# Kernel optimization log

Hardware: AMD Instinct MI355X
Metric: run time of the kernel (lower is better)

Reference implementation:

```python
import jax, jax.numpy as jnp
import numpy as np

IN_C, HID, OUT = 3, 128, 256
K1, K2 = 16, 8
N = 8192


def _knn_idx(x, k):
    # x: [N, C] -> indices of k nearest neighbors (excluding self), [N, k]
    n = x.shape[0]
    sq = jnp.sum(x * x, axis=1)
    d = sq[:, None] + sq[None, :] - 2.0 * (x @ x.T)  # [N, N] squared dists
    i = jnp.arange(n)
    d = d.at[i, i].set(jnp.inf)  # loop=False: exclude self
    _, idx = jax.lax.top_k(-d, k)
    return idx


def _edge_conv(x, W1, b1, W2, b2, k):
    # DynamicEdgeConv: knn graph on x, edge feat [x_i, x_j - x_i], MLP, max aggr
    n, c = x.shape
    idx = _knn_idx(x, k)              # [N, k]
    xj = x[idx]                       # [N, k, C]
    xi = x[:, None, :]                # [N, 1, C]
    e = jnp.concatenate([jnp.broadcast_to(xi, (n, k, c)), xj - xi], axis=-1)  # [N, k, 2C]
    h = jax.nn.relu(e @ W1 + b1) @ W2 + b2  # [N, k, H]
    return jnp.max(h, axis=1)               # max aggregation -> [N, H]


def setup_inputs() -> dict:
    key = jax.random.key(0)
    ks = jax.random.split(key, 9)
    def lin(k, fan_in, fan_out):
        bound = 1.0 / np.sqrt(fan_in)
        kw, kb = jax.random.split(k)
        W = jax.random.uniform(kw, (fan_in, fan_out), jnp.float32, -bound, bound)
        b = jax.random.uniform(kb, (fan_out,), jnp.float32, -bound, bound)
        return W, b
    x = jax.random.normal(ks[0], (N, IN_C), jnp.float32)
    W1a, b1a = lin(ks[1], 2 * IN_C, HID)
    W1b, b1b = lin(ks[2], HID, HID)
    W2a, b2a = lin(ks[3], 2 * HID, OUT)
    W2b, b2b = lin(ks[4], OUT, OUT)
    return {"x": x, "W1a": W1a, "b1a": b1a, "W1b": W1b, "b1b": b1b,
            "W2a": W2a, "b2a": b2a, "W2b": W2b, "b2b": b2b}


def reference(x, W1a, b1a, W1b, b1b, W2a, b2a, W2b, b2b):
    h = _edge_conv(x, W1a, b1a, W1b, b1b, K1)   # [N, HID]
    out = _edge_conv(h, W2a, b2a, W2b, b2b, K2)  # [N, OUT]
    return out
```

## Files before the change

### kernel.cpp

```cpp
#include <hip/hip_runtime.h>
#include <math.h>

constexpr int NPTS  = 8192;
constexpr int HIDC  = 128;
constexpr int OUTC2 = 256;
constexpr int PQC   = 512;
constexpr int KK1   = 16;
constexpr int KK2   = 8;

typedef __attribute__((ext_vector_type(8))) short short8;
typedef __attribute__((ext_vector_type(4))) float f32x4;

__device__ __forceinline__ f32x4 mfma16(short8 a, short8 b, f32x4 c) {
  return __builtin_amdgcn_mfma_f32_16x16x32_bf16(a, b, c, 0, 0, 0);
}

__device__ __forceinline__ void async_ld16(void* lds, const void* g) {
  __builtin_amdgcn_global_load_lds(
      (const __attribute__((address_space(1))) unsigned int*)g,
      (__attribute__((address_space(3))) unsigned int*)lds, 16, 0, 0);
}

#define CEU(a, b) { unsigned _t = (a) < (b) ? (a) : (b); (b) = (a) < (b) ? (b) : (a); (a) = _t; }

__device__ __forceinline__ void topk8_batch4(unsigned (&kk)[KK2],
                                             unsigned b0, unsigned b1,
                                             unsigned b2, unsigned b3) {
  CEU(b0, b1); CEU(b2, b3); CEU(b0, b2); CEU(b1, b3); CEU(b1, b2);
  if (b0 < kk[7]) {
    kk[4] = kk[4] < b3 ? kk[4] : b3;
    kk[5] = kk[5] < b2 ? kk[5] : b2;
    kk[6] = kk[6] < b1 ? kk[6] : b1;
    kk[7] = kk[7] < b0 ? kk[7] : b0;
    CEU(kk[0], kk[4]); CEU(kk[1], kk[5]); CEU(kk[2], kk[6]); CEU(kk[3], kk[7]);
    CEU(kk[0], kk[2]); CEU(kk[1], kk[3]); CEU(kk[4], kk[6]); CEU(kk[5], kk[7]);
    CEU(kk[0], kk[1]); CEU(kk[2], kk[3]); CEU(kk[4], kk[5]); CEU(kk[6], kk[7]);
  }
}

template <int K>
__device__ __forceinline__ void ins_lex(float (&kf)[K], int (&ki)[K], float v, int j) {
  bool ins = (v < kf[K - 1]) || (v == kf[K - 1] && j < ki[K - 1]);
  if (ins) {
    kf[K - 1] = v; ki[K - 1] = j;
    #pragma unroll
    for (int p = K - 1; p > 0; --p) {
      float fa = kf[p - 1], fb = kf[p];
      int   ia = ki[p - 1], ib = ki[p];
      bool sw = (fb < fa) || (fb == fa && ib < ia);
      kf[p - 1] = sw ? fb : fa; ki[p - 1] = sw ? ib : ia;
      kf[p]     = sw ? fa : fb; ki[p]     = sw ? ia : ib;
    }
  }
}

__device__ __forceinline__ unsigned short bf16_rn(float x) {
  unsigned int u = __float_as_uint(x);
  unsigned int r = u + 0x7fffu + ((u >> 16) & 1u);
  return (unsigned short)(r >> 16);
}

__global__ void pack_x_kernel(const float* __restrict__ x, float4* __restrict__ x4) {
  int i = blockIdx.x * blockDim.x + threadIdx.x;
  if (i < NPTS) {
    float a = x[3 * i], b = x[3 * i + 1], c = x[3 * i + 2];
    x4[i] = make_float4(a, b, c, a * a + b * b + c * c);
  }
}

__global__ void prep_w1f_kernel(const float* __restrict__ W1,
                                unsigned short* __restrict__ WcFhi,
                                unsigned short* __restrict__ WcFlo) {
  int idx = blockIdx.x * 256 + threadIdx.x;
  int k = idx >> 9, c = idx & 511;
  float wh = W1[(size_t)(HIDC + k) * OUTC2 + (c & 255)];
  float w = (c < OUTC2) ? (W1[(size_t)k * OUTC2 + c] - wh) : wh;
  unsigned short hi = bf16_rn(w);
  float fh = __uint_as_float(((unsigned int)hi) << 16);
  unsigned short lo = bf16_rn(w - fh);
  const int nt = c >> 4, ct = c & 15;
  const int s = k >> 5, kg = (k >> 3) & 3, e = k & 7;
  const size_t fidx = ((size_t)(s * 32 + nt) * 64 + (kg * 16 + ct)) * 8 + e;
  WcFhi[fidx] = hi;
  WcFlo[fidx] = lo;
}

__global__ void prep_w1b_kernel(const float* __restrict__ W,
                                unsigned short* __restrict__ Fhi,
                                unsigned short* __restrict__ Flo) {
  const int c = blockIdx.x;
  const int k = threadIdx.x;
  float w = W[(size_t)k * HIDC + c];
  unsigned short hi = bf16_rn(w);
  float fh = __uint_as_float(((unsigned int)hi) << 16);
  unsigned short lo = bf16_rn(w - fh);
  const int nt = c >> 4, ct = c & 15;
  const int s = k >> 5, kg = (k >> 3) & 3, e = k & 7;
  const size_t idx = ((size_t)(s * 8 + nt) * 64 + (kg * 16 + ct)) * 8 + e;
  Fhi[idx] = hi;
  Flo[idx] = lo;
}

__global__ void prep_w2_kernel(const float* __restrict__ W2,
                               unsigned short* __restrict__ W2Fhi,
                               unsigned short* __restrict__ W2Flo) {
  const int c = blockIdx.x;
  const int k = threadIdx.x;
  float w = W2[(size_t)k * OUTC2 + c];
  unsigned short hi = bf16_rn(w);
  float fh = __uint_as_float(((unsigned int)hi) << 16);
  unsigned short lo = bf16_rn(w - fh);
  const int nt = c >> 4, ct = c & 15;
  const int s  = k >> 5, kg = (k >> 3) & 3, e = k & 7;
  const int lane = kg * 16 + ct;
  const size_t idx = ((size_t)(s * 16 + nt) * 64 + lane) * 8 + e;
  W2Fhi[idx] = hi;
  W2Flo[idx] = lo;
}

__global__ __launch_bounds__(256) void knn3_kernel(const float4* __restrict__ X4,
                                                   int* __restrict__ idx_out) {
  const int tid  = threadIdx.x;
  const int lane = tid & 63;
  const int wv   = __builtin_amdgcn_readfirstlane(tid >> 6);
  const int qA   = blockIdx.x * 8 + wv * 2;
  const int qB   = qA + 1;

  const float4 qa = X4[qA];
  const float4 qb = X4[qB];

  unsigned kkA[KK2], kkB[KK2];
  #pragma unroll
  for (int k = 0; k < KK2; ++k) { kkA[k] = 0xFFFFFFFFu; kkB[k] = 0xFFFFFFFFu; }

  for (int c = 0; c < NPTS / 256; ++c) {
    const int j = c * 256 + lane * 4;
    float4 p[4];
    #pragma unroll
    for (int t = 0; t < 4; ++t) p[t] = X4[j + t];

    unsigned ka[4], kb[4];
    #pragma unroll
    for (int t = 0; t < 4; ++t) {
      float dA = fmaxf(qa.w + p[t].w - 2.f * (qa.x * p[t].x + qa.y * p[t].y + qa.z * p[t].z), 0.f);
      float dB = fmaxf(qb.w + p[t].w - 2.f * (qb.x * p[t].x + qb.y * p[t].y + qb.z * p[t].z), 0.f);
      ka[t] = (__float_as_uint(dA) & 0xFFFFE000u) | (unsigned)(j + t);
      kb[t] = (__float_as_uint(dB) & 0xFFFFE000u) | (unsigned)(j + t);
      if (j + t == qA) ka[t] = 0xFFFFFFFFu;
      if (j + t == qB) kb[t] = 0xFFFFFFFFu;
    }
    topk8_batch4(kkA, ka[0], ka[1], ka[2], ka[3]);
    topk8_batch4(kkB, kb[0], kb[1], kb[2], kb[3]);
  }

  float kfA[KK2], kfB[KK2]; int kjA[KK2], kjB[KK2];
  #pragma unroll
  for (int k = 0; k < KK2; ++k) {
    kfA[k] = INFINITY; kjA[k] = 0x7fffffff;
    kfB[k] = INFINITY; kjB[k] = 0x7fffffff;
  }
  #pragma unroll
  for (int k = 0; k < KK2; ++k) {
    int j = (int)(kkA[k] & 0x1FFFu);
    float4 pj = X4[j];
    float d = qa.w + pj.w - 2.f * (qa.x * pj.x + qa.y * pj.y + qa.z * pj.z);
    if (kkA[k] == 0xFFFFFFFFu) { d = INFINITY; j = 0x7fffffff; }
    ins_lex<KK2>(kfA, kjA, d, j);
  }
  #pragma unroll
  for (int k = 0; k < KK2; ++k) {
    int j = (int)(kkB[k] & 0x1FFFu);
    float4 pj = X4[j];
    float d = qb.w + pj.w - 2.f * (qb.x * pj.x + qb.y * pj.y + qb.z * pj.z);
    if (kkB[k] == 0xFFFFFFFFu) { d = INFINITY; j = 0x7fffffff; }
    ins_lex<KK2>(kfB, kjB, d, j);
  }

  #pragma unroll
  for (int k = 0; k < KK1; ++k) {
    float mf = kfA[0]; int mj = kjA[0];
    #pragma unroll
    for (int m = 1; m <= 32; m <<= 1) {
      float of = __shfl_xor(mf, m, 64);
      int   oj = __shfl_xor(mj, m, 64);
      bool g = (of < mf) || (of == mf && oj < mj);
      mf = g ? of : mf; mj = g ? oj : mj;
    }
    const bool won = (kfA[0] == mf) && (kjA[0] == mj);
    if (won) {
      idx_out[(size_t)qA * KK1 + k] = mj;
      #pragma unroll
      for (int p = 0; p < KK2 - 1; ++p) { kfA[p] = kfA[p + 1]; kjA[p] = kjA[p + 1]; }
      kfA[KK2 - 1] = INFINITY; kjA[KK2 - 1] = 0x7fffffff;
    }
  }
  #pragma unroll
  for (int k = 0; k < KK1; ++k) {
    float mf = kfB[0]; int mj = kjB[0];
    #pragma unroll
    for (int m = 1; m <= 32; m <<= 1) {
      float of = __shfl_xor(mf, m, 64);
      int   oj = __shfl_xor(mj, m, 64);
      bool g = (of < mf) || (of == mf && oj < mj);
      mf = g ? of : mf; mj = g ? oj : mj;
    }
    const bool won = (kfB[0] == mf) && (kjB[0] == mj);
    if (won) {
      idx_out[(size_t)qB * KK1 + k] = mj;
      #pragma unroll
      for (int p = 0; p < KK2 - 1; ++p) { kfB[p] = kfB[p + 1]; kjB[p] = kjB[p + 1]; }
      kfB[KK2 - 1] = INFINITY; kjB[KK2 - 1] = 0x7fffffff;
    }
  }
}

__global__ __launch_bounds__(512) void edgeconv1_kernel(
    const float* __restrict__ X, const int* __restrict__ knn,
    const float* __restrict__ W1, const float* __restrict__ b1,
    const unsigned short* __restrict__ W1bFhi, const unsigned short* __restrict__ W1bFlo,
    const float* __restrict__ b2,
    float* __restrict__ H, unsigned short* __restrict__ Hhi,
    unsigned short* __restrict__ Hlo, float* __restrict__ SQ2) {
  __shared__ __align__(16) unsigned short Ghi[128 * HIDC];
  __shared__ __align__(16) unsigned short Glo[128 * HIDC];
  __shared__ __align__(16) unsigned short Bs[2][2][4096];
  __shared__ float xjs[8][KK1][3];
  __shared__ float xis[8][3];
  const int tid  = threadIdx.x;
  const int lane = tid & 63;
  const int wv   = __builtin_amdgcn_readfirstlane(tid >> 6);
  const int p    = blockIdx.x * 8 + wv;

  if (lane < KK1) {
    int j = knn[p * KK1 + lane];
    xjs[wv][lane][0] = X[3 * j]; xjs[wv][lane][1] = X[3 * j + 1]; xjs[wv][lane][2] = X[3 * j + 2];
  } else if (lane < KK1 + 3) {
    xis[wv][lane - KK1] = X[3 * p + lane - KK1];
  }
  __syncthreads();

  {
    const int ch0 = lane * 2;
    float2 w1r[6];
    #pragma unroll
    for (int c = 0; c < 6; ++c)
      w1r[c] = make_float2(W1[c * HIDC + ch0], W1[c * HIDC + ch0 + 1]);
    const float2 b1v = make_float2(b1[ch0], b1[ch0 + 1]);
    const float xi0 = xis[wv][0], xi1 = xis[wv][1], xi2 = xis[wv][2];
    const float base0 = b1v.x + xi0 * w1r[0].x + xi1 * w1r[1].x + xi2 * w1r[2].x;
    const float base1 = b1v.y + xi0 * w1r[0].y + xi1 * w1r[1].y + xi2 * w1r[2].y;
    #pragma unroll
    for (int e = 0; e < KK1; ++e) {
      float dx = xjs[wv][e][0] - xi0, dy = xjs[wv][e][1] - xi1, dz = xjs[wv][e][2] - xi2;
      float v0 = fmaxf(base0 + dx * w1r[3].x + dy * w1r[4].x + dz * w1r[5].x, 0.f);
      float v1 = fmaxf(base1 + dx * w1r[3].y + dy * w1r[4].y + dz * w1r[5].y, 0.f);
      unsigned short h0 = bf16_rn(v0), h1s = bf16_rn(v1);
      unsigned short l0 = bf16_rn(v0 - __uint_as_float(((unsigned)h0) << 16));
      unsigned short l1 = bf16_rn(v1 - __uint_as_float(((unsigned)h1s) << 16));
      const int r   = wv * 16 + e;
      const int off = r * 256 + (((ch0 >> 3) ^ (r & 7)) << 4) + ((ch0 & 7) << 1);
      *(ushort2*)((char*)Ghi + off) = make_ushort2(h0, h1s);
      *(ushort2*)((char*)Glo + off) = make_ushort2(l0, l1);
    }
  }

  auto stageB = [&](int buf, int s) {
    const size_t go = (size_t)s * 4096 + (size_t)wv * 512 + (size_t)lane * 8;
    async_ld16((char*)&Bs[buf][0][0] + wv * 1024, W1bFhi + go);
    async_ld16((char*)&Bs[buf][1][0] + wv * 1024, W1bFlo + go);
  };

  stageB(0, 0);
  asm volatile("s_waitcnt vmcnt(0)" ::: "memory");
  __syncthreads();

  const int col = lane & 15;
  const int kg  = lane >> 4;
  const int ar  = wv * 16 + col;
  const int abase = ar * 256;

  f32x4 acc[8];
  #pragma unroll
  for (int n = 0; n < 8; ++n) acc[n] = (f32x4){0.f, 0.f, 0.f, 0.f};

  for (int s = 0; s < 4; ++s) {
    const int cur = s & 1;
    if (s + 1 < 4) stageB(cur ^ 1, s + 1);
    const int asl = (((s * 4 + kg) ^ (ar & 7)) << 4);
    short8 ghi = *(const short8*)((const char*)Ghi + abase + asl);
    short8 glo = *(const short8*)((const char*)Glo + abase + asl);
    #pragma unroll
    for (int n = 0; n < 8; ++n) {
      const int bo = (n * 64 + lane) * 16;
      short8 bhi = *(const short8*)((const char*)&Bs[cur][0][0] + bo);
      short8 blo = *(const short8*)((const char*)&Bs[cur][1][0] + bo);
      acc[n] = mfma16(ghi, bhi, acc[n]);
      acc[n] = mfma16(ghi, blo, acc[n]);
      acc[n] = mfma16(glo, bhi, acc[n]);
    }
    asm volatile("s_waitcnt vmcnt(0)" ::: "memory");
    __syncthreads();
  }

  float sq = 0.f;
  float hv[8];
  #pragma unroll
  for (int n = 0; n < 8; ++n) {
    float m = fmaxf(fmaxf(acc[n][0], acc[n][1]), fmaxf(acc[n][2], acc[n][3]));
    m = fmaxf(m, __shfl_xor(m, 16, 64));
    m = fmaxf(m, __shfl_xor(m, 32, 64));
    m += b2[n * 16 + col];
    hv[n] = m;
    sq += m * m;
  }
  if (kg == 0) {
    #pragma unroll
    for (int n = 0; n < 8; ++n) {
      const int ch = n * 16 + col;
      H[(size_t)p * HIDC + ch] = hv[n];
      unsigned short hb = bf16_rn(hv[n]);
      float fh = __uint_as_float(((unsigned)hb) << 16);
      Hhi[(size_t)p * HIDC + ch] = hb;
      Hlo[(size_t)p * HIDC + ch] = bf16_rn(hv[n] - fh);
    }
  }
  #pragma unroll
  for (int m2 = 1; m2 <= 8; m2 <<= 1) sq += __shfl_xor(sq, m2, 64);
  if (lane == 0) SQ2[p] = sq;
}

__global__ __launch_bounds__(512) void gemm_pq_kernel(
    const unsigned short* __restrict__ Hhi, const unsigned short* __restrict__ Hlo,
    const unsigned short* __restrict__ WcFhi, const unsigned short* __restrict__ WcFlo,
    const float* __restrict__ b1, float* __restrict__ PQ) {
  __shared__ __align__(16) unsigned short Ahi[64 * HIDC];
  __shared__ __align__(16) unsigned short Alo[64 * HIDC];
  __shared__ __align__(16) unsigned short Bsl[2][2][8192];
  const int tid  = threadIdx.x;
  const int lane = tid & 63;
  const int wv   = __builtin_amdgcn_readfirstlane(tid >> 6);
  const int mb   = blockIdx.x >> 1;
  const int ns   = blockIdx.x & 1;
  const int r0   = mb * 64;

  #pragma unroll
  for (int i = 0; i < 2; ++i) {
    const int srow = wv * 8 + i * 4 + (lane >> 4);
    const int sslt = (lane & 15) ^ (srow & 7);
    const size_t go = (size_t)(r0 + srow) * HIDC + sslt * 8;
    async_ld16((char*)Ahi + (wv * 8 + i * 4) * 256, Hhi + go);
    async_ld16((char*)Alo + (wv * 8 + i * 4) * 256, Hlo + go);
  }
  auto stageB = [&](int buf, int s) {
    #pragma unroll
    for (int i = 0; i < 2; ++i) {
      const size_t go = (size_t)(s * 32 + ns * 16) * 512 + (size_t)wv * 1024 + i * 512 + lane * 8;
      async_ld16((char*)&Bsl[buf][0][0] + wv * 2048 + i * 1024, WcFhi + go);
      async_ld16((char*)&Bsl[buf][1][0] + wv * 2048 + i * 1024, WcFlo + go);
    }
  };
  stageB(0, 0);
  asm volatile("s_waitcnt vmcnt(0)" ::: "memory");
  __syncthreads();

  const int col = lane & 15;
  const int kg  = lane >> 4;
  const int mt  = wv & 3;
  const int nh  = wv >> 2;
  const int ar  = mt * 16 + col;
  const int abase = ar * 256;

  f32x4 acc[8];
  #pragma unroll
  for (int n = 0; n < 8; ++n) acc[n] = (f32x4){0.f, 0.f, 0.f, 0.f};

  for (int s = 0; s < 4; ++s) {
    const int cur = s & 1;
    if (s + 1 < 4) stageB(cur ^ 1, s + 1);
    const int asl = (((s * 4 + kg) ^ (ar & 7)) << 4);
    short8 ahi8 = *(const short8*)((const char*)Ahi + abase + asl);
    short8 alo8 = *(const short8*)((const char*)Alo + abase + asl);
    #pragma unroll
    for (int n = 0; n < 8; ++n) {
      const int ntl = nh * 8 + n;
      const int bo = (ntl * 64 + lane) * 16;
      short8 bhi = *(const short8*)((const char*)&Bsl[cur][0][0] + bo);
      short8 blo = *(const short8*)((const char*)&Bsl[cur][1][0] + bo);
      acc[n] = mfma16(ahi8, bhi, acc[n]);
      acc[n] = mfma16(ahi8, blo, acc[n]);
      acc[n] = mfma16(alo8, bhi, acc[n]);
    }
    asm volatile("s_waitcnt vmcnt(0)" ::: "memory");
    __syncthreads();
  }

  #pragma unroll
  for (int n = 0; n < 8; ++n) {
    const int cg = ns * 256 + (nh * 8 + n) * 16 + col;
    const float bb = (ns == 0) ? b1[cg] : 0.f;
    #pragma unroll
    for (int r = 0; r < 4; ++r) {
      const int row = r0 + mt * 16 + kg * 4 + r;
      PQ[(size_t)row * PQC + cg] = acc[n][r] + bb;
    }
  }
}

constexpr int JSPLIT = 16;
constexpr int JPB2   = NPTS / JSPLIT;
constexpr int NCH    = JPB2 / 16;
constexpr int CPQ    = JSPLIT * KK2;

__global__ __launch_bounds__(256) void knn128_filter_kernel(
    const unsigned short* __restrict__ Hhi, const unsigned short* __restrict__ Hlo,
    const float* __restrict__ SQ, unsigned* __restrict__ pk2) {
  __shared__ __align__(16) unsigned short As[2][2][16 * HIDC];
  const int tid  = threadIdx.x;
  const int lane = tid & 63;
  const int wv   = __builtin_amdgcn_readfirstlane(tid >> 6);
  const int qb   = blockIdx.x >> 4;
  const int js   = blockIdx.x & 15;
  const int col  = lane & 15;
  const int kg   = lane >> 4;
  const int qg   = qb * 64 + wv * 16 + col;

  short8 qhi[4], qlo[4];
  #pragma unroll
  for (int s = 0; s < 4; ++s) {
    const size_t o = (size_t)qg * HIDC + s * 32 + kg * 8;
    qhi[s] = *reinterpret_cast<const short8*>(Hhi + o);
    qlo[s] = *reinterpret_cast<const short8*>(Hlo + o);
  }
  const float sqq = SQ[qg];

  unsigned kk[KK2];
  #pragma unroll
  for (int k = 0; k < KK2; ++k) kk[k] = 0xFFFFFFFFu;

  const int jbase = js * JPB2;

  const int srow = 4 * wv + (lane >> 4);
  const int sslt = (lane & 15) ^ (srow & 7);
  auto stage = [&](int buf, int ch) {
    const size_t gofs = (size_t)(jbase + ch * 16 + srow) * HIDC + sslt * 8;
    async_ld16((char*)&As[buf][0][0] + wv * 1024, Hhi + gofs);
    async_ld16((char*)&As[buf][1][0] + wv * 1024, Hlo + gofs);
  };

  stage(0, 0);
  asm volatile("s_waitcnt vmcnt(0)" ::: "memory");
  __syncthreads();

  for (int ch = 0; ch < NCH; ++ch) {
    const int cur = ch & 1;
    if (ch + 1 < NCH) stage(cur ^ 1, ch + 1);

    const int jb = jbase + ch * 16;
    short8 ahi[4], alo[4];
    const int rowb = col * 256;
    #pragma unroll
    for (int s = 0; s < 4; ++s) {
      const int sl = ((s * 4 + kg) ^ (col & 7)) * 16;
      ahi[s] = *(const short8*)((const char*)&As[cur][0][0] + rowb + sl);
      alo[s] = *(const short8*)((const char*)&As[cur][1][0] + rowb + sl);
    }
    f32x4 sqjv = *reinterpret_cast<const f32x4*>(SQ + jb + kg * 4);

    f32x4 acc = {0.f, 0.f, 0.f, 0.f};
    #pragma unroll
    for (int s = 0; s < 4; ++s) {
      acc = mfma16(ahi[s], qhi[s], acc);
      acc = mfma16(ahi[s], qlo[s], acc);
      acc = mfma16(alo[s], qhi[s], acc);
    }
    unsigned kb[4];
    #pragma unroll
    for (int r = 0; r < 4; ++r) {
      const int jg = jb + kg * 4 + r;
      float d = fmaxf(sqq + sqjv[r] - 2.f * acc[r], 0.f);
      kb[r] = (__float_as_uint(d) & 0xFFFFE000u) | (unsigned)jg;
      if (jg == qg) kb[r] = 0xFFFFFFFFu;
    }
    topk8_batch4(kk, kb[0], kb[1], kb[2], kb[3]);
    asm volatile("s_waitcnt vmcnt(0)" ::: "memory");
    __syncthreads();
  }

  #pragma unroll
  for (int dlt = 16; dlt <= 32; dlt <<= 1) {
    unsigned ok[KK2];
    #pragma unroll
    for (int k = 0; k < KK2; ++k) ok[k] = __shfl_xor((int)kk[k], dlt, 64);
    topk8_batch4(kk, ok[0], ok[1], ok[2], ok[3]);
    topk8_batch4(kk, ok[4], ok[5], ok[6], ok[7]);
  }
  if (lane < 16) {
    const size_t base = (size_t)qg * CPQ + js * KK2;
    #pragma unroll
    for (int k = 0; k < KK2; ++k) pk2[base + k] = kk[k];
  }
}

__global__ __launch_bounds__(256) void knn_rescore_kernel(
    const float* __restrict__ H, const float* __restrict__ SQ,
    const unsigned* __restrict__ pk2, int* __restrict__ idx_out) {
  __shared__ float qrow[16][HIDC + 4];
  const int tid  = threadIdx.x;
  const int lane = tid & 63;
  const int wv   = tid >> 6;
  const int g    = lane >> 4;
  const int sl   = lane & 15;
  const int q0   = blockIdx.x * 16;
  const int qloc = wv * 4 + g;
  const int q    = q0 + qloc;

  for (int u = tid; u < 16 * 32; u += 256) {
    int r = u >> 5, c4 = u & 31;
    *(f32x4*)&qrow[r][c4 * 4] = *(const f32x4*)&H[(size_t)(q0 + r) * HIDC + c4 * 4];
  }
  __syncthreads();

  unsigned kreg[KK2];
  {
    const unsigned* src = pk2 + (size_t)q * CPQ + sl * KK2;
    uint4 a = *(const uint4*)(src);
    uint4 b = *(const uint4*)(src + 4);
    kreg[0] = a.x; kreg[1] = a.y; kreg[2] = a.z; kreg[3] = a.w;
    kreg[4] = b.x; kreg[5] = b.y; kreg[6] = b.z; kreg[7] = b.w;
  }

  unsigned ckey = 0xFFFFFFFFu;
  #pragma unroll
  for (int t = 0; t < 16; ++t) {
    unsigned m = kreg[0];
    #pragma unroll
    for (int mm = 1; mm <= 8; mm <<= 1) {
      unsigned o = (unsigned)__shfl_xor((int)m, mm, 64);
      m = o < m ? o : m;
    }
    if (t == sl) ckey = m;
    const bool won = (kreg[0] == m);
    if (won) {
      #pragma unroll
      for (int p = 0; p < KK2 - 1; ++p) kreg[p] = kreg[p + 1];
      kreg[KK2 - 1] = 0xFFFFFFFFu;
    }
  }
  const int ci = (int)(ckey & 0x1FFFu);

  const float* crow = H + (size_t)ci * HIDC;
  float dot = 0.f;
  #pragma unroll 8
  for (int c4 = 0; c4 < HIDC / 4; ++c4) {
    f32x4 qv = *(const f32x4*)&qrow[qloc][c4 * 4];
    f32x4 cv = *(const f32x4*)(crow + c4 * 4);
    dot += qv[0] * cv[0] + qv[1] * cv[1] + qv[2] * cv[2] + qv[3] * cv[3];
  }
  float d = SQ[q] + SQ[ci] - 2.f * dot;

  float kf[KK2]; int ki[KK2];
  kf[0] = d; ki[0] = ci;
  #pragma unroll
  for (int k = 1; k < KK2; ++k) { kf[k] = INFINITY; ki[k] = 0x7fffffff; }
  #pragma unroll
  for (int dlt = 1; dlt <= 8; dlt <<= 1) {
    float of[KK2]; int oi[KK2];
    #pragma unroll
    for (int k = 0; k < KK2; ++k) { of[k] = __shfl_xor(kf[k], dlt, 64); oi[k] = __shfl_xor(ki[k], dlt, 64); }
    #pragma unroll
    for (int k = 0; k < KK2; ++k) ins_lex<KK2>(kf, ki, of[k], oi[k]);
  }
  if (sl == 0) {
    #pragma unroll
    for (int k = 0; k < KK2; ++k) idx_out[(size_t)q * KK2 + k] = ki[k];
  }
}

__global__ __launch_bounds__(512) void edgeconv2_kernel(
    const float* __restrict__ PQ, const int* __restrict__ knn,
    const unsigned short* __restrict__ W2Fhi, const unsigned short* __restrict__ W2Flo,
    const float* __restrict__ b2, float* __restrict__ Out) {
  __shared__ __align__(16) unsigned short Ghi[64 * OUTC2];
  __shared__ __align__(16) unsigned short Glo[64 * OUTC2];
  __shared__ __align__(16) unsigned short Bs[2][2][8192];
  const int tid  = threadIdx.x;
  const int lane = tid & 63;
  const int wv   = __builtin_amdgcn_readfirstlane(tid >> 6);
  const int p_base = blockIdx.x * 8;

  {
    const int p   = p_base + wv;
    const int ch0 = lane * 4;
    f32x4 pv = *(const f32x4*)&PQ[(size_t)p * PQC + ch0];
    #pragma unroll
    for (int e = 0; e < KK2; ++e) {
      const int j = knn[p * KK2 + e];
      f32x4 qv = *(const f32x4*)&PQ[(size_t)j * PQC + OUTC2 + ch0];
      unsigned short hb[4], lb[4];
      #pragma unroll
      for (int c = 0; c < 4; ++c) {
        float g = fmaxf(pv[c] + qv[c], 0.f);
        hb[c] = bf16_rn(g);
        float fh = __uint_as_float(((unsigned int)hb[c]) << 16);
        lb[c] = bf16_rn(g - fh);
      }
      const int r   = wv * 8 + e;
      const int off = r * 512 + (((ch0 >> 3) ^ (r & 7)) << 4) + ((ch0 & 7) << 1);
      *(ushort4*)((char*)Ghi + off) = make_ushort4(hb[0], hb[1], hb[2], hb[3]);
      *(ushort4*)((char*)Glo + off) = make_ushort4(lb[0], lb[1], lb[2], lb[3]);
    }
  }

  auto stageB = [&](int buf, int s) {
    #pragma unroll
    for (int i = 0; i < 2; ++i) {
      const size_t go = (size_t)s * 8192 + (size_t)(wv * 2 + i) * 512 + (size_t)lane * 8;
      async_ld16((char*)&Bs[buf][0][0] + (wv * 2 + i) * 1024, W2Fhi + go);
      async_ld16((char*)&Bs[buf][1][0] + (wv * 2 + i) * 1024, W2Flo + go);
    }
  };

  stageB(0, 0);
  asm volatile("s_waitcnt vmcnt(0)" ::: "memory");
  __syncthreads();

  const int col = lane & 15;
  const int kg  = lane >> 4;
  const int mt  = wv & 3;
  const int nh  = wv >> 2;
  const int ar  = mt * 16 + col;
  const int abase = ar * 512;

  f32x4 acc[8];
  #pragma unroll
  for (int n = 0; n < 8; ++n) acc[n] = (f32x4){0.f, 0.f, 0.f, 0.f};

  for (int s = 0; s < 8; ++s) {
    const int cur = s & 1;
    if (s + 1 < 8) stageB(cur ^ 1, s + 1);

    const int asl = (((s * 4 + kg) ^ (ar & 7)) << 4);
    short8 ghi = *(const short8*)((const char*)Ghi + abase + asl);
    short8 glo = *(const short8*)((const char*)Glo + abase + asl);
    #pragma unroll
    for (int n = 0; n < 8; ++n) {
      const int nt = nh * 8 + n;
      const int bo = (nt * 64 + lane) * 16;
      short8 bhi = *(const short8*)((const char*)&Bs[cur][0][0] + bo);
      short8 blo = *(const short8*)((const char*)&Bs[cur][1][0] + bo);
      acc[n] = mfma16(ghi, bhi, acc[n]);
      acc[n] = mfma16(ghi, blo, acc[n]);
      acc[n] = mfma16(glo, bhi, acc[n]);
    }
    asm volatile("s_waitcnt vmcnt(0)" ::: "memory");
    __syncthreads();
  }

  const int pt = p_base + mt * 2 + (kg >> 1);
  #pragma unroll
  for (int n = 0; n < 8; ++n) {
    float m = fmaxf(fmaxf(acc[n][0], acc[n][1]), fmaxf(acc[n][2], acc[n][3]));
    m = fmaxf(m, __shfl_xor(m, 16, 64));
    if ((kg & 1) == 0) {
      const int ncol = nh * 128 + n * 16 + col;
      Out[(size_t)pt * OUTC2 + ncol] = m + b2[ncol];
    }
  }
}

extern "C" void kernel_launch(void* const* d_in, const int* in_sizes, int n_in,
                              void* d_out, int out_size, void* d_ws, size_t ws_size,
                              hipStream_t stream) {
  const float* x   = (const float*)d_in[0];
  const float* W1a = (const float*)d_in[1];
  const float* b1a = (const float*)d_in[2];
  const float* W1b = (const float*)d_in[3];
  const float* b1b = (const float*)d_in[4];
  const float* W2a = (const float*)d_in[5];
  const float* b2a = (const float*)d_in[6];
  const float* W2b = (const float*)d_in[7];
  const float* b2b = (const float*)d_in[8];
  float* out = (float*)d_out;

  float* h    = (float*)d_ws;
  float* sq2  = h + (size_t)NPTS * HIDC;
  int*   idx1 = (int*)(sq2 + NPTS);
  int*   idx2 = idx1 + (size_t)NPTS * KK1;
  unsigned short* Hhi = (unsigned short*)(idx2 + (size_t)NPTS * KK2);
  unsigned short* Hlo = Hhi + (size_t)NPTS * HIDC;
  unsigned* pk2 = (unsigned*)(Hlo + (size_t)NPTS * HIDC);
  float* PQ   = (float*)(pk2 + (size_t)NPTS * CPQ);
  unsigned short* W2Fhi = (unsigned short*)(PQ + (size_t)NPTS * PQC);
  unsigned short* W2Flo = W2Fhi + (size_t)OUTC2 * OUTC2;
  unsigned short* WcFhi = W2Flo + (size_t)OUTC2 * OUTC2;
  unsigned short* WcFlo = WcFhi + (size_t)HIDC * PQC;
  unsigned short* W1bFhi = WcFlo + (size_t)HIDC * PQC;
  unsigned short* W1bFlo = W1bFhi + (size_t)HIDC * HIDC;
  float4* x4 = (float4*)h;

  pack_x_kernel<<<(NPTS + 255) / 256, 256, 0, stream>>>(x, x4);
  prep_w1f_kernel<<<(HIDC * PQC) / 256, 256, 0, stream>>>(W2a, WcFhi, WcFlo);
  prep_w1b_kernel<<<HIDC, HIDC, 0, stream>>>(W1b, W1bFhi, W1bFlo);
  prep_w2_kernel<<<OUTC2, OUTC2, 0, stream>>>(W2b, W2Fhi, W2Flo);
  knn3_kernel<<<NPTS / 8, 256, 0, stream>>>(x4, idx1);
  edgeconv1_kernel<<<NPTS / 8, 512, 0, stream>>>(x, idx1, W1a, b1a,
                                                 W1bFhi, W1bFlo, b1b,
                                                 h, Hhi, Hlo, sq2);
  gemm_pq_kernel<<<(NPTS / 64) * 2, 512, 0, stream>>>(Hhi, Hlo, WcFhi, WcFlo, b2a, PQ);
  knn128_filter_kernel<<<(NPTS / 64) * JSPLIT, 256, 0, stream>>>(Hhi, Hlo, sq2, pk2);
  knn_rescore_kernel<<<NPTS / 16, 256, 0, stream>>>(h, sq2, pk2, idx2);
  edgeconv2_kernel<<<NPTS / 8, 512, 0, stream>>>(PQ, idx2, W2Fhi, W2Flo, b2b, out);
}
```

Before: 263.1 us.

## Merge weight prep kernels, batch-8 top-k in knn3, 32-row chunks in knn128 filter

Folds the three weight-preparation kernels into one launch to cut launch overhead. knn3 now processes eight candidates per lane per iteration and uses a sorting network plus a bitonic merge (topk8_batch8) instead of two batch-4 inserts. knn128_filter stages 32 rows per LDS chunk, halving barriers and waits, and its cross-lane reduction merges already-sorted lists directly. The costs are more registers in knn3 and double the LDS in the filter kernel, which may lower occupancy.

```diff
diff --git a/kernel.cpp b/kernel.cpp
--- a/kernel.cpp
+++ b/kernel.cpp
@@ -22,6 +22,32 @@
 }
 
 #define CEU(a, b) { unsigned _t = (a) < (b) ? (a) : (b); (b) = (a) < (b) ? (b) : (a); (a) = _t; }
+
+__device__ __forceinline__ void topk8_merge_sorted(unsigned (&kk)[KK2], unsigned (&b)[KK2]) {
+  if (b[0] < kk[7]) {
+    kk[0] = kk[0] < b[7] ? kk[0] : b[7];
+    kk[1] = kk[1] < b[6] ? kk[1] : b[6];
+    kk[2] = kk[2] < b[5] ? kk[2] : b[5];
+    kk[3] = kk[3] < b[4] ? kk[3] : b[4];
+    kk[4] = kk[4] < b[3] ? kk[4] : b[3];
+    kk[5] = kk[5] < b[2] ? kk[5] : b[2];
+    kk[6] = kk[6] < b[1] ? kk[6] : b[1];
+    kk[7] = kk[7] < b[0] ? kk[7] : b[0];
+    CEU(kk[0], kk[4]); CEU(kk[1], kk[5]); CEU(kk[2], kk[6]); CEU(kk[3], kk[7]);
+    CEU(kk[0], kk[2]); CEU(kk[1], kk[3]); CEU(kk[4], kk[6]); CEU(kk[5], kk[7]);
+    CEU(kk[0], kk[1]); CEU(kk[2], kk[3]); CEU(kk[4], kk[5]); CEU(kk[6], kk[7]);
+  }
+}
+
+__device__ __forceinline__ void topk8_batch8(unsigned (&kk)[KK2], unsigned (&b)[KK2]) {
+  CEU(b[0], b[1]); CEU(b[2], b[3]); CEU(b[4], b[5]); CEU(b[6], b[7]);
+  CEU(b[0], b[2]); CEU(b[1], b[3]); CEU(b[4], b[6]); CEU(b[5], b[7]);
+  CEU(b[1], b[2]); CEU(b[5], b[6]);
+  CEU(b[0], b[4]); CEU(b[1], b[5]); CEU(b[2], b[6]); CEU(b[3], b[7]);
+  CEU(b[2], b[4]); CEU(b[3], b[5]);
+  CEU(b[1], b[2]); CEU(b[3], b[4]); CEU(b[5], b[6]);
+  topk8_merge_sorted(kk, b);
+}
 
 __device__ __forceinline__ void topk8_batch4(unsigned (&kk)[KK2],
                                              unsigned b0, unsigned b1,
@@ -68,54 +94,54 @@
   }
 }
 
-__global__ void prep_w1f_kernel(const float* __restrict__ W1,
-                                unsigned short* __restrict__ WcFhi,
-                                unsigned short* __restrict__ WcFlo) {
-  int idx = blockIdx.x * 256 + threadIdx.x;
-  int k = idx >> 9, c = idx & 511;
-  float wh = W1[(size_t)(HIDC + k) * OUTC2 + (c & 255)];
-  float w = (c < OUTC2) ? (W1[(size_t)k * OUTC2 + c] - wh) : wh;
-  unsigned short hi = bf16_rn(w);
-  float fh = __uint_as_float(((unsigned int)hi) << 16);
-  unsigned short lo = bf16_rn(w - fh);
-  const int nt = c >> 4, ct = c & 15;
-  const int s = k >> 5, kg = (k >> 3) & 3, e = k & 7;
-  const size_t fidx = ((size_t)(s * 32 + nt) * 64 + (kg * 16 + ct)) * 8 + e;
-  WcFhi[fidx] = hi;
-  WcFlo[fidx] = lo;
-}
-
-__global__ void prep_w1b_kernel(const float* __restrict__ W,
-                                unsigned short* __restrict__ Fhi,
-                                unsigned short* __restrict__ Flo) {
-  const int c = blockIdx.x;
-  const int k = threadIdx.x;
-  float w = W[(size_t)k * HIDC + c];
-  unsigned short hi = bf16_rn(w);
-  float fh = __uint_as_float(((unsigned int)hi) << 16);
-  unsigned short lo = bf16_rn(w - fh);
-  const int nt = c >> 4, ct = c & 15;
-  const int s = k >> 5, kg = (k >> 3) & 3, e = k & 7;
-  const size_t idx = ((size_t)(s * 8 + nt) * 64 + (kg * 16 + ct)) * 8 + e;
-  Fhi[idx] = hi;
-  Flo[idx] = lo;
-}
-
-__global__ void prep_w2_kernel(const float* __restrict__ W2,
-                               unsigned short* __restrict__ W2Fhi,
-                               unsigned short* __restrict__ W2Flo) {
-  const int c = blockIdx.x;
-  const int k = threadIdx.x;
-  float w = W2[(size_t)k * OUTC2 + c];
-  unsigned short hi = bf16_rn(w);
-  float fh = __uint_as_float(((unsigned int)hi) << 16);
-  unsigned short lo = bf16_rn(w - fh);
-  const int nt = c >> 4, ct = c & 15;
-  const int s  = k >> 5, kg = (k >> 3) & 3, e = k & 7;
-  const int lane = kg * 16 + ct;
-  const size_t idx = ((size_t)(s * 16 + nt) * 64 + lane) * 8 + e;
-  W2Fhi[idx] = hi;
-  W2Flo[idx] = lo;
+__global__ void prep_weights_kernel(
+    const float* __restrict__ W2a, const float* __restrict__ W1b,
+    const float* __restrict__ W2b,
+    unsigned short* __restrict__ WcFhi, unsigned short* __restrict__ WcFlo,
+    unsigned short* __restrict__ W1bFhi, unsigned short* __restrict__ W1bFlo,
+    unsigned short* __restrict__ W2Fhi, unsigned short* __restrict__ W2Flo) {
+  const int blk = blockIdx.x;
+  const int tid = threadIdx.x;
+  if (blk < 256) {
+    int idx = blk * 256 + tid;
+    int k = idx >> 9, c = idx & 511;
+    float wh = W2a[(size_t)(HIDC + k) * OUTC2 + (c & 255)];
+    float w = (c < OUTC2) ? (W2a[(size_t)k * OUTC2 + c] - wh) : wh;
+    unsigned short hi = bf16_rn(w);
+    float fh = __uint_as_float(((unsigned int)hi) << 16);
+    unsigned short lo = bf16_rn(w - fh);
+    const int nt = c >> 4, ct = c & 15;
+    const int s = k >> 5, kg = (k >> 3) & 3, e = k & 7;
+    const size_t fidx = ((size_t)(s * 32 + nt) * 64 + (kg * 16 + ct)) * 8 + e;
+    WcFhi[fidx] = hi;
+    WcFlo[fidx] = lo;
+  } else if (blk < 384) {
+    if (tid < HIDC) {
+      const int c = blk - 256;
+      const int k = tid;
+      float w = W1b[(size_t)k * HIDC + c];
+      unsigned short hi = bf16_rn(w);
+      float fh = __uint_as_float(((unsigned int)hi) << 16);
+      unsigned short lo = bf16_rn(w - fh);
+      const int nt = c >> 4, ct = c & 15;
+      const int s = k >> 5, kg = (k >> 3) & 3, e = k & 7;
+      const size_t idx = ((size_t)(s * 8 + nt) * 64 + (kg * 16 + ct)) * 8 + e;
+      W1bFhi[idx] = hi;
+      W1bFlo[idx] = lo;
+    }
+  } else {
+    const int c = blk - 384;
+    const int k = tid;
+    float w = W2b[(size_t)k * OUTC2 + c];
+    unsigned short hi = bf16_rn(w);
+    float fh = __uint_as_float(((unsigned int)hi) << 16);
+    unsigned short lo = bf16_rn(w - fh);
+    const int nt = c >> 4, ct = c & 15;
+    const int s  = k >> 5, kg = (k >> 3) & 3, e = k & 7;
+    const size_t idx = ((size_t)(s * 16 + nt) * 64 + (kg * 16 + ct)) * 8 + e;
+    W2Fhi[idx] = hi;
+    W2Flo[idx] = lo;
+  }
 }
 
 __global__ __launch_bounds__(256) void knn3_kernel(const float4* __restrict__ X4,
@@ -133,15 +159,15 @@
   #pragma unroll
   for (int k = 0; k < KK2; ++k) { kkA[k] = 0xFFFFFFFFu; kkB[k] = 0xFFFFFFFFu; }
 
-  for (int c = 0; c < NPTS / 256; ++c) {
-    const int j = c * 256 + lane * 4;
-    float4 p[4];
-    #pragma unroll
-    for (int t = 0; t < 4; ++t) p[t] = X4[j + t];
-
-    unsigned ka[4], kb[4];
-    #pragma unroll
-    for (int t = 0; t < 4; ++t) {
+  for (int c = 0; c < NPTS / 512; ++c) {
+    const int j = c * 512 + lane * 8;
+    float4 p[8];
+    #pragma unroll
+    for (int t = 0; t < 8; ++t) p[t] = X4[j + t];
+
+    unsigned ka[KK2], kb[KK2];
+    #pragma unroll
+    for (int t = 0; t < 8; ++t) {
       float dA = fmaxf(qa.w + p[t].w - 2.f * (qa.x * p[t].x + qa.y * p[t].y + qa.z * p[t].z), 0.f);
       float dB = fmaxf(qb.w + p[t].w - 2.f * (qb.x * p[t].x + qb.y * p[t].y + qb.z * p[t].z), 0.f);
       ka[t] = (__float_as_uint(dA) & 0xFFFFE000u) | (unsigned)(j + t);
@@ -149,8 +175,8 @@
       if (j + t == qA) ka[t] = 0xFFFFFFFFu;
       if (j + t == qB) kb[t] = 0xFFFFFFFFu;
     }
-    topk8_batch4(kkA, ka[0], ka[1], ka[2], ka[3]);
-    topk8_batch4(kkB, kb[0], kb[1], kb[2], kb[3]);
+    topk8_batch8(kkA, ka);
+    topk8_batch8(kkB, kb);
   }
 
   float kfA[KK2], kfB[KK2]; int kjA[KK2], kjB[KK2];
@@ -408,13 +434,13 @@
 
 constexpr int JSPLIT = 16;
 constexpr int JPB2   = NPTS / JSPLIT;
-constexpr int NCH    = JPB2 / 16;
+constexpr int NCH2   = JPB2 / 32;
 constexpr int CPQ    = JSPLIT * KK2;
 
 __global__ __launch_bounds__(256) void knn128_filter_kernel(
     const unsigned short* __restrict__ Hhi, const unsigned short* __restrict__ Hlo,
     const float* __restrict__ SQ, unsigned* __restrict__ pk2) {
-  __shared__ __align__(16) unsigned short As[2][2][16 * HIDC];
+  __shared__ __align__(16) unsigned short As[2][2][32 * HIDC];
   const int tid  = threadIdx.x;
   const int lane = tid & 63;
   const int wv   = __builtin_amdgcn_readfirstlane(tid >> 6);
@@ -439,49 +465,55 @@
 
   const int jbase = js * JPB2;
 
-  const int srow = 4 * wv + (lane >> 4);
-  const int sslt = (lane & 15) ^ (srow & 7);
   auto stage = [&](int buf, int ch) {
-    const size_t gofs = (size_t)(jbase + ch * 16 + srow) * HIDC + sslt * 8;
-    async_ld16((char*)&As[buf][0][0] + wv * 1024, Hhi + gofs);
-    async_ld16((char*)&As[buf][1][0] + wv * 1024, Hlo + gofs);
+    #pragma unroll
+    for (int i = 0; i < 2; ++i) {
+      const int srow = 8 * wv + i * 4 + (lane >> 4);
+      const int sslt = (lane & 15) ^ (srow & 7);
+      const size_t gofs = (size_t)(jbase + ch * 32 + srow) * HIDC + sslt * 8;
+      async_ld16((char*)&As[buf][0][0] + (8 * wv + i * 4) * 256, Hhi + gofs);
+      async_ld16((char*)&As[buf][1][0] + (8 * wv + i * 4) * 256, Hlo + gofs);
+    }
   };
 
   stage(0, 0);
   asm volatile("s_waitcnt vmcnt(0)" ::: "memory");
   __syncthreads();
 
-  for (int ch = 0; ch < NCH; ++ch) {
+  for (int ch = 0; ch < NCH2; ++ch) {
     const int cur = ch & 1;
-    if (ch + 1 < NCH) stage(cur ^ 1, ch + 1);
-
-    const int jb = jbase + ch * 16;
-    short8 ahi[4], alo[4];
-    const int rowb = col * 256;
-    #pragma unroll
-    for (int s = 0; s < 4; ++s) {
-      const int sl = ((s * 4 + kg) ^ (col & 7)) * 16;
-      ahi[s] = *(const short8*)((const char*)&As[cur][0][0] + rowb + sl);
-      alo[s] = *(const short8*)((const char*)&As[cur][1][0] + rowb + sl);
-    }
-    f32x4 sqjv = *reinterpret_cast<const f32x4*>(SQ + jb + kg * 4);
-
-    f32x4 acc = {0.f, 0.f, 0.f, 0.f};
-    #pragma unroll
-    for (int s = 0; s < 4; ++s) {
-      acc = mfma16(ahi[s], qhi[s], acc);
-      acc = mfma16(ahi[s], qlo[s], acc);
-      acc = mfma16(alo[s], qhi[s], acc);
-    }
-    unsigned kb[4];
-    #pragma unroll
-    for (int r = 0; r < 4; ++r) {
-      const int jg = jb + kg * 4 + r;
-      float d = fmaxf(sqq + sqjv[r] - 2.f * acc[r], 0.f);
-      kb[r] = (__float_as_uint(d) & 0xFFFFE000u) | (unsigned)jg;
-      if (jg == qg) kb[r] = 0xFFFFFFFFu;
-    }
-    topk8_batch4(kk, kb[0], kb[1], kb[2], kb[3]);
+    if (ch + 1 < NCH2) stage(cur ^ 1, ch + 1);
+
+    #pragma unroll
+    for (int t = 0; t < 2; ++t) {
+      const int jb = jbase + ch * 32 + t * 16;
+      short8 ahi[4], alo[4];
+      const int rowb = (t * 16 + col) * 256;
+      #pragma unroll
+      for (int s = 0; s < 4; ++s) {
+        const int sl = ((s * 4 + kg) ^ (col & 7)) * 16;
+        ahi[s] = *(const short8*)((const char*)&As[cur][0][0] + rowb + sl);
+        alo[s] = *(const short8*)((const char*)&As[cur][1][0] + rowb + sl);
+      }
+      f32x4 sqjv = *reinterpret_cast<const f32x4*>(SQ + jb + kg * 4);
+
+      f32x4 acc = {0.f, 0.f, 0.f, 0.f};
+      #pragma unroll
+      for (int s = 0; s < 4; ++s) {
+        acc = mfma16(ahi[s], qhi[s], acc);
+        acc = mfma16(ahi[s], qlo[s], acc);
+        acc = mfma16(alo[s], qhi[s], acc);
+      }
+      unsigned kb[4];
+      #pragma unroll
+      for (int r = 0; r < 4; ++r) {
+        const int jg = jb + kg * 4 + r;
+        float d = fmaxf(sqq + sqjv[r] - 2.f * acc[r], 0.f);
+        kb[r] = (__float_as_uint(d) & 0xFFFFE000u) | (unsigned)jg;
+        if (jg == qg) kb[r] = 0xFFFFFFFFu;
+      }
+      topk8_batch4(kk, kb[0], kb[1], kb[2], kb[3]);
+    }
     asm volatile("s_waitcnt vmcnt(0)" ::: "memory");
     __syncthreads();
   }
@@ -491,8 +523,7 @@
     unsigned ok[KK2];
     #pragma unroll
     for (int k = 0; k < KK2; ++k) ok[k] = __shfl_xor((int)kk[k], dlt, 64);
-    topk8_batch4(kk, ok[0], ok[1], ok[2], ok[3]);
-    topk8_batch4(kk, ok[4], ok[5], ok[6], ok[7]);
+    topk8_merge_sorted(kk, ok);
   }
   if (lane < 16) {
     const size_t base = (size_t)qg * CPQ + js * KK2;
@@ -699,9 +730,9 @@
   float4* x4 = (float4*)h;
 
   pack_x_kernel<<<(NPTS + 255) / 256, 256, 0, stream>>>(x, x4);
-  prep_w1f_kernel<<<(HIDC * PQC) / 256, 256, 0, stream>>>(W2a, WcFhi, WcFlo);
-  prep_w1b_kernel<<<HIDC, HIDC, 0, stream>>>(W1b, W1bFhi, W1bFlo);
-  prep_w2_kernel<<<OUTC2, OUTC2, 0, stream>>>(W2b, W2Fhi, W2Flo);
+  prep_weights_kernel<<<640, 256, 0, stream>>>(W2a, W1b, W2b,
+                                               WcFhi, WcFlo, W1bFhi, W1bFlo,
+                                               W2Fhi, W2Flo);
   knn3_kernel<<<NPTS / 8, 256, 0, stream>>>(x4, idx1);
   edgeconv1_kernel<<<NPTS / 8, 512, 0, stream>>>(x, idx1, W1a, b1a,
                                                  W1bFhi, W1bFlo, b1b,
```

Result: slower. 285.4 us (+8.5%).
